# Optimization experiments

Measured on AMD Instinct MI355X. Metric: run time of the kernel, lower is better.

## Reference

```python
import jax, jax.numpy as jnp
import numpy as np

L, D, H, FF, V = 8, 768, 8, 2048, 32000
MAXLEN, TMAX = 512, 4
S = MAXLEN * TMAX  # 2048 context length
HD = D // H
EPS = 1e-4  # layer_norm_eps from module defaults


def setup_inputs() -> dict:
    key = jax.random.key(0)
    ks = jax.random.split(key, 16)
    s = 0.02
    B = 1
    rn = lambda k, shape: jax.random.normal(k, shape, jnp.float32) * s
    # sinusoidal positional encoding over MAXLEN real-token positions
    pos = np.arange(MAXLEN)[:, None]
    div = np.exp(np.arange(0, D, 2) * (-np.log(10000.0) / D))
    pe = np.zeros((MAXLEN, D), np.float32)
    pe[:, 0::2] = np.sin(pos * div)
    pe[:, 1::2] = np.cos(pos * div)
    return {
        "state_embeddings": jax.random.normal(ks[0], (B, S, D), jnp.float32),
        "padding_mask": jnp.zeros((B, S), bool),
        "pe": jnp.asarray(pe),
        "thought_emb": rn(ks[1], (TMAX, D)),
        "w_qkv": rn(ks[2], (L, 3 * D, D)),
        "b_qkv": jnp.zeros((L, 3 * D), jnp.float32),
        "w_out": rn(ks[3], (L, D, D)),
        "b_out": jnp.zeros((L, D), jnp.float32),
        "ln1_g": jnp.ones((L, D), jnp.float32),
        "ln1_b": jnp.zeros((L, D), jnp.float32),
        "ln2_g": jnp.ones((L, D), jnp.float32),
        "ln2_b": jnp.zeros((L, D), jnp.float32),
        "w_ff1": rn(ks[4], (L, FF, D)),
        "b_ff1": jnp.zeros((L, FF), jnp.float32),
        "w_ff2": rn(ks[5], (L, D, FF)),
        "b_ff2": jnp.zeros((L, D), jnp.float32),
        "fn_g": jnp.ones((D,), jnp.float32),
        "fn_b": jnp.zeros((D,), jnp.float32),
        "w_policy": rn(ks[6], (V, D)),
        "w_v1": rn(ks[7], (FF, D)),
        "b_v1": jnp.zeros((FF,), jnp.float32),
        "w_v2": rn(ks[8], (1, FF)),
        "b_v2": jnp.zeros((1,), jnp.float32),
        "n_thoughts_taken": 3,
    }


def _layer_norm(x, g, b):
    m = x.mean(-1, keepdims=True)
    v = ((x - m) ** 2).mean(-1, keepdims=True)
    return (x - m) / jnp.sqrt(v + EPS) * g + b


def reference(state_embeddings, padding_mask, pe, thought_emb, w_qkv, b_qkv, w_out, b_out, ln1_g, ln1_b, ln2_g, ln2_b, w_ff1, b_ff1, w_ff2, b_ff2, fn_g, fn_b, w_policy, w_v1, b_v1, w_v2, b_v2, n_thoughts_taken):
    tt = int(n_thoughts_taken)
    T = tt + 1  # block size (token + thoughts taken)
    B = state_embeddings.shape[0]
    R = MAXLEN  # real_token_count: all token slots real (no padding)
    # --- DualPositionalEncoding ---
    x = state_embeddings[:, :MAXLEN * T].reshape(B, MAXLEN, T, D)
    x = x + pe[None, :, None, :] + thought_emb[None, None, :T, :]
    x = x.reshape(B, MAXLEN * T, D)
    x = jnp.pad(x, ((0, 0), (0, S - MAXLEN * T), (0, 0)))
    # --- ThoughtsFormer block-causal mask (keep=True means attend) ---
    i = jnp.arange(S)
    tok, off = i // T, i % T
    same_block = (tok[:, None] == tok[None, :]) & (off[:, None] >= off[None, :]) & (tok[:, None] < R)
    global_cols = (off[None, :] == 0) & (tok[None, :] < R) & (i[:, None] > i[None, :]) & (i[:, None] < R * T)
    keep = (same_block | global_cols)[None, None] & (~padding_mask)[:, None, None, :]
    scale = 1.0 / np.sqrt(HD)

    def layer(h, p):
        wq, bq, wo, bo, g1, b1, g2, b2, wf1, bf1, wf2, bf2 = p
        # pre-norm self-attention
        y = _layer_norm(h, g1, b1)
        q, k, v = jnp.split(y @ wq.T + bq, 3, axis=-1)
        q = q.reshape(B, S, H, HD)
        k = k.reshape(B, S, H, HD)
        v = v.reshape(B, S, H, HD)
        scores = jnp.einsum('bihd,bjhd->bhij', q, k) * scale
        attn = jax.nn.softmax(jnp.where(keep, scores, -jnp.inf), axis=-1)
        o = jnp.einsum('bhij,bjhd->bihd', attn, v).reshape(B, S, D)
        h = h + o @ wo.T + bo
        # pre-norm FFN with exact (erf) GELU
        y = _layer_norm(h, g2, b2)
        h = h + jax.nn.gelu(y @ wf1.T + bf1, approximate=False) @ wf2.T + bf2
        h = jnp.where(jnp.isnan(h), 0.0, h)
        return h, None

    x, _ = jax.lax.scan(layer, x, (w_qkv, b_qkv, w_out, b_out, ln1_g, ln1_b, ln2_g, ln2_b, w_ff1, b_ff1, w_ff2, b_ff2))
    x = _layer_norm(x, fn_g, fn_b)  # TransformerEncoder final norm
    logits = x @ w_policy.T  # policy head (no bias)
    values = jax.nn.gelu(x @ w_v1.T + b_v1, approximate=False) @ w_v2.T + b_v2
    return logits, values
```

## Files before the change

### kernel.cpp

```cpp
#include <hip/hip_runtime.h>
#include <math.h>

#define S_TOT 2048
#define DMODEL 768
#define QKVD 2304
#define NHEAD 8
#define HDIM 96
#define FFDIM 2048
#define VOCAB 32000
#define MAXLEN_C 512
#define POL_CHUNK 3200
#define VLT_LD 2080
#define NEG_BIG (-3.0e38f)
#define M_INIT (-1.0e30f)
#define QK_SCALE 0.10206207261596575f

typedef __bf16 bf16x8 __attribute__((ext_vector_type(8)));
typedef float f32x4 __attribute__((ext_vector_type(4)));
typedef unsigned short u16x8 __attribute__((ext_vector_type(8)));
typedef unsigned short u16x4 __attribute__((ext_vector_type(4)));

__device__ __forceinline__ float gelu_exact(float x) {
  return 0.5f * x * (1.0f + erff(x * 0.70710678118654752f));
}

__device__ __forceinline__ float bf2f(unsigned short u) {
  union { unsigned int i; float f; } v;
  v.i = ((unsigned int)u) << 16;
  return v.f;
}

__device__ __forceinline__ unsigned short f2bf(float f) {
  union { float f; unsigned int i; } v;
  v.f = f;
  unsigned int x = v.i;
  return (unsigned short)((x + 0x7fffu + ((x >> 16) & 1u)) >> 16);
}

__device__ __forceinline__ unsigned int pack2bf(float a, float b) {
  return (unsigned int)f2bf(a) | ((unsigned int)f2bf(b) << 16);
}

__device__ __forceinline__ void gload_lds16(const unsigned short* g, unsigned short* l) {
  __builtin_amdgcn_global_load_lds(
      (const __attribute__((address_space(1))) unsigned int*)g,
      (__attribute__((address_space(3))) unsigned int*)l, 16, 0, 0);
}

__global__ __launch_bounds__(256) void embed_kernel(
    const float* __restrict__ se, const float* __restrict__ pe,
    const float* __restrict__ th, const int* __restrict__ ntt,
    float* __restrict__ X) {
  int idx = blockIdx.x * 256 + threadIdx.x;
  if (idx >= S_TOT * DMODEL) return;
  int p = idx / DMODEL;
  int d = idx - p * DMODEL;
  int T = ntt[0] + 1;
  float v = 0.0f;
  if (p < MAXLEN_C * T) {
    v = se[idx] + pe[(p / T) * DMODEL + d] + th[(p % T) * DMODEL + d];
  }
  X[idx] = v;
}

__global__ __launch_bounds__(256) void ln_bf_kernel(
    const float* __restrict__ X, const float* __restrict__ g,
    const float* __restrict__ b, unsigned short* __restrict__ Y) {
  __shared__ float red[4];
  const int row = blockIdx.x;
  const int tid = threadIdx.x;
  const float* x = X + (size_t)row * DMODEL;
  float v0 = x[tid], v1 = x[tid + 256], v2 = x[tid + 512];
  float s = v0 + v1 + v2;
  for (int o = 32; o; o >>= 1) s += __shfl_xor(s, o);
  if ((tid & 63) == 0) red[tid >> 6] = s;
  __syncthreads();
  float mean = (red[0] + red[1] + red[2] + red[3]) * (1.0f / DMODEL);
  float d0 = v0 - mean, d1 = v1 - mean, d2 = v2 - mean;
  float s2 = d0 * d0 + d1 * d1 + d2 * d2;
  for (int o = 32; o; o >>= 1) s2 += __shfl_xor(s2, o);
  __syncthreads();
  if ((tid & 63) == 0) red[tid >> 6] = s2;
  __syncthreads();
  float var = (red[0] + red[1] + red[2] + red[3]) * (1.0f / DMODEL);
  float rstd = rsqrtf(var + 1e-4f);
  unsigned short* y = Y + (size_t)row * DMODEL;
  y[tid]       = f2bf(d0 * rstd * g[tid]       + b[tid]);
  y[tid + 256] = f2bf(d1 * rstd * g[tid + 256] + b[tid + 256]);
  y[tid + 512] = f2bf(d2 * rstd * g[tid + 512] + b[tid + 512]);
}

__global__ __launch_bounds__(256) void cvt_kernel(
    const float* __restrict__ s, unsigned short* __restrict__ d, int n) {
  int i = (blockIdx.x * 256 + threadIdx.x) * 4;
  if (i >= n) return;
  float4 v = *(const float4*)(s + i);
  u16x4 o;
  o[0] = f2bf(v.x); o[1] = f2bf(v.y); o[2] = f2bf(v.z); o[3] = f2bf(v.w);
  *(u16x4*)(d + i) = o;
}

__global__ __launch_bounds__(256) void cvt4_kernel(
    const float* __restrict__ s0, const float* __restrict__ s1,
    const float* __restrict__ s2, const float* __restrict__ s3,
    unsigned short* __restrict__ d0, unsigned short* __restrict__ d1,
    unsigned short* __restrict__ d2, unsigned short* __restrict__ d3,
    int n0, int n1, int n2, int n3) {
  int i = (blockIdx.x * 256 + threadIdx.x) * 4;
  const float* s;
  unsigned short* d;
  if (i < n0) { s = s0; d = d0; }
  else if (i < n0 + n1) { i -= n0; s = s1; d = d1; }
  else if (i < n0 + n1 + n2) { i -= n0 + n1; s = s2; d = d2; }
  else if (i < n0 + n1 + n2 + n3) { i -= n0 + n1 + n2; s = s3; d = d3; }
  else return;
  float4 v = *(const float4*)(s + i);
  u16x4 o;
  o[0] = f2bf(v.x); o[1] = f2bf(v.y); o[2] = f2bf(v.z); o[3] = f2bf(v.w);
  *(u16x4*)(d + i) = o;
}

__global__ __launch_bounds__(256) void cvt6_kernel(
    const float* __restrict__ s0, const float* __restrict__ s1,
    const float* __restrict__ s2, const float* __restrict__ s3,
    const float* __restrict__ s4, const float* __restrict__ s5,
    unsigned short* __restrict__ d0, unsigned short* __restrict__ d1,
    unsigned short* __restrict__ d2, unsigned short* __restrict__ d3,
    unsigned short* __restrict__ d4, unsigned short* __restrict__ d5,
    int n0, int n1, int n2, int n3, int n4, int n5) {
  int i = (blockIdx.x * 256 + threadIdx.x) * 4;
  const float* s;
  unsigned short* d;
  if (i < n0) { s = s0; d = d0; }
  else if (i < n0 + n1) { i -= n0; s = s1; d = d1; }
  else if (i < n0 + n1 + n2) { i -= n0 + n1; s = s2; d = d2; }
  else if (i < n0 + n1 + n2 + n3) { i -= n0 + n1 + n2; s = s3; d = d3; }
  else if (i < n0 + n1 + n2 + n3 + n4) { i -= n0 + n1 + n2 + n3; s = s4; d = d4; }
  else if (i < n0 + n1 + n2 + n3 + n4 + n5) { i -= n0 + n1 + n2 + n3 + n4; s = s5; d = d5; }
  else return;
  float4 v = *(const float4*)(s + i);
  u16x4 o;
  o[0] = f2bf(v.x); o[1] = f2bf(v.y); o[2] = f2bf(v.z); o[3] = f2bf(v.w);
  *(u16x4*)(d + i) = o;
}

__global__ __launch_bounds__(256) void gemm_bf16_kernel(
    const unsigned short* __restrict__ A, const unsigned short* __restrict__ B,
    const float* __restrict__ bias, const float* __restrict__ res,
    void* __restrict__ Cout, int M, int N, int K, int ldc, int act, int outbf,
    int swiz) {
  __shared__ __align__(16) unsigned short As[2 * 4096];
  __shared__ __align__(16) unsigned short Bs[2 * 4096];
  const int t = threadIdx.x;
  const int w = t >> 6, l = t & 63;
  int n_blk, m_blk;
  if (swiz) {
    const int g = blockIdx.x;
    const int chunk = gridDim.x >> 3;
    const int logical = (g & 7) * chunk + (g >> 3);
    m_blk = logical & 15;
    n_blk = logical >> 4;
  } else {
    n_blk = blockIdx.x; m_blk = blockIdx.y;
  }
  const int n0 = n_blk * 128, i0 = m_blk * 128;
  const int wr = w >> 1, wc = w & 1;
  const int lr = l & 15;
  const int koff = (l >> 4) * 8;

  f32x4 acc[4][4] = {};

  const int srow = t >> 2;
  const int scol = (t & 3) * 8;
  const unsigned short* Ag = A + (size_t)(i0 + srow) * K + scol;
  const unsigned short* Bg = B + (size_t)(n0 + srow) * K + scol;
  const int lo0 = (w << 9);
  const int lo1 = 2048 + (w << 9);

#define STAGE128(buf, k0)                                        \
  do {                                                           \
    gload_lds16(Ag + (k0), &As[(buf) * 4096 + lo0]);             \
    gload_lds16(Ag + (size_t)64 * K + (k0), &As[(buf) * 4096 + lo1]); \
    gload_lds16(Bg + (k0), &Bs[(buf) * 4096 + lo0]);             \
    gload_lds16(Bg + (size_t)64 * K + (k0), &Bs[(buf) * 4096 + lo1]); \
  } while (0)

#define COMPUTE128(buf)                                                   \
  do {                                                                    \
    const unsigned short* Ab = &As[(buf) * 4096];                         \
    const unsigned short* Bb = &Bs[(buf) * 4096];                         \
    bf16x8 af[4], bfr[4];                                                 \
    _Pragma("unroll") for (int fi = 0; fi < 4; ++fi)                      \
        af[fi] = *(const bf16x8*)&Ab[(wr * 64 + fi * 16 + lr) * 32 + koff]; \
    _Pragma("unroll") for (int fj = 0; fj < 4; ++fj)                      \
        bfr[fj] = *(const bf16x8*)&Bb[(wc * 64 + fj * 16 + lr) * 32 + koff]; \
    _Pragma("unroll") for (int fi = 0; fi < 4; ++fi)                      \
      _Pragma("unroll") for (int fj = 0; fj < 4; ++fj)                    \
          acc[fi][fj] = __builtin_amdgcn_mfma_f32_16x16x32_bf16(          \
              bfr[fj], af[fi], acc[fi][fj], 0, 0, 0);                     \
  } while (0)

  const int nt = K >> 5;
  STAGE128(0, 0);
  int cur = 0;
  for (int tt = 0; tt < nt - 1; ++tt) {
    STAGE128(cur ^ 1, (tt + 1) << 5);
    asm volatile("s_waitcnt vmcnt(4)" ::: "memory");
    __builtin_amdgcn_s_barrier();
    __builtin_amdgcn_sched_barrier(0);
    COMPUTE128(cur);
    __builtin_amdgcn_sched_barrier(0);
    __builtin_amdgcn_s_barrier();
    cur ^= 1;
  }
  asm volatile("s_waitcnt vmcnt(0)" ::: "memory");
  __builtin_amdgcn_s_barrier();
  __builtin_amdgcn_sched_barrier(0);
  COMPUTE128(cur);

  const int mloc = l & 15, ng = (l >> 4) * 4;
#pragma unroll
  for (int fi = 0; fi < 4; ++fi) {
    const int i = i0 + wr * 64 + fi * 16 + mloc;
    const size_t rowbase = (size_t)i * ldc;
#pragma unroll
    for (int fj = 0; fj < 4; ++fj) {
      const int nb = n0 + wc * 64 + fj * 16 + ng;
      float z0 = acc[fi][fj][0], z1 = acc[fi][fj][1];
      float z2 = acc[fi][fj][2], z3 = acc[fi][fj][3];
      if (bias) {
        float4 bv = *(const float4*)(bias + nb);
        z0 += bv.x; z1 += bv.y; z2 += bv.z; z3 += bv.w;
      }
      if (act) {
        z0 = gelu_exact(z0); z1 = gelu_exact(z1);
        z2 = gelu_exact(z2); z3 = gelu_exact(z3);
      }
      if (res) {
        float4 rv = *(const float4*)(res + rowbase + nb);
        z0 += rv.x; z1 += rv.y; z2 += rv.z; z3 += rv.w;
      }
      if (outbf) {
        u16x4 o;
        o[0] = f2bf(z0); o[1] = f2bf(z1); o[2] = f2bf(z2); o[3] = f2bf(z3);
        *(u16x4*)((unsigned short*)Cout + rowbase + nb) = o;
      } else {
        *(float4*)((float*)Cout + rowbase + nb) = make_float4(z0, z1, z2, z3);
      }
    }
  }
#undef STAGE128
#undef COMPUTE128
}

__global__ __launch_bounds__(256) void gemm64_bf16_kernel(
    const unsigned short* __restrict__ A, const unsigned short* __restrict__ B,
    const float* __restrict__ bias, const float* __restrict__ res,
    void* __restrict__ Cout, int M, int N, int K, int ldc, int act, int outbf) {
  __shared__ __align__(16) unsigned short As[2 * 4096];
  __shared__ __align__(16) unsigned short Bs[2 * 4096];
  const int t = threadIdx.x;
  const int w = t >> 6, l = t & 63;
  const int n0 = blockIdx.x * 64, i0 = blockIdx.y * 64;
  const int wr = w >> 1, wc = w & 1;
  const int lr = l & 15;
  const int koff = (l >> 4) * 8;

  f32x4 acc[2][2] = {};

  const int srow = t >> 2;
  const int scol = (t & 3) * 8;
  const unsigned short* Ag = A + (size_t)(i0 + srow) * K + scol;
  const unsigned short* Bg = B + (size_t)(n0 + srow) * K + scol;
  const int lo0 = (w << 9);
  const int lo1 = 2048 + (w << 9);

#define STAGE64(buf, k0)                                      \
  do {                                                        \
    gload_lds16(Ag + (k0), &As[(buf) * 4096 + lo0]);          \
    gload_lds16(Ag + (k0) + 32, &As[(buf) * 4096 + lo1]);     \
    gload_lds16(Bg + (k0), &Bs[(buf) * 4096 + lo0]);          \
    gload_lds16(Bg + (k0) + 32, &Bs[(buf) * 4096 + lo1]);     \
  } while (0)

#define COMPUTE64(buf)                                                        \
  do {                                                                        \
    const unsigned short* Ab = &As[(buf) * 4096];                             \
    const unsigned short* Bb = &Bs[(buf) * 4096];                             \
    bf16x8 af[2][2], bfr[2][2];                                               \
    _Pragma("unroll") for (int fi = 0; fi < 2; ++fi)                          \
      _Pragma("unroll") for (int kk = 0; kk < 2; ++kk)                        \
          af[fi][kk] = *(const bf16x8*)&Ab[kk * 2048 + (wr * 32 + fi * 16 + lr) * 32 + koff]; \
    _Pragma("unroll") for (int fj = 0; fj < 2; ++fj)                          \
      _Pragma("unroll") for (int kk = 0; kk < 2; ++kk)                        \
          bfr[fj][kk] = *(const bf16x8*)&Bb[kk * 2048 + (wc * 32 + fj * 16 + lr) * 32 + koff]; \
    _Pragma("unroll") for (int fi = 0; fi < 2; ++fi)                          \
      _Pragma("unroll") for (int fj = 0; fj < 2; ++fj)                        \
        _Pragma("unroll") for (int kk = 0; kk < 2; ++kk)                      \
            acc[fi][fj] = __builtin_amdgcn_mfma_f32_16x16x32_bf16(            \
                bfr[fj][kk], af[fi][kk], acc[fi][fj], 0, 0, 0);               \
  } while (0)

  const int nt = K >> 6;
  STAGE64(0, 0);
  int cur = 0;
  for (int tt = 0; tt < nt - 1; ++tt) {
    STAGE64(cur ^ 1, (tt + 1) << 6);
    asm volatile("s_waitcnt vmcnt(4)" ::: "memory");
    __builtin_amdgcn_s_barrier();
    __builtin_amdgcn_sched_barrier(0);
    COMPUTE64(cur);
    __builtin_amdgcn_sched_barrier(0);
    __builtin_amdgcn_s_barrier();
    cur ^= 1;
  }
  asm volatile("s_waitcnt vmcnt(0)" ::: "memory");
  __builtin_amdgcn_s_barrier();
  __builtin_amdgcn_sched_barrier(0);
  COMPUTE64(cur);

  const int mloc = l & 15, ng = (l >> 4) * 4;
#pragma unroll
  for (int fi = 0; fi < 2; ++fi) {
    const int i = i0 + wr * 32 + fi * 16 + mloc;
    const size_t rowbase = (size_t)i * ldc;
#pragma unroll
    for (int fj = 0; fj < 2; ++fj) {
      const int nb = n0 + wc * 32 + fj * 16 + ng;
      float z0 = acc[fi][fj][0], z1 = acc[fi][fj][1];
      float z2 = acc[fi][fj][2], z3 = acc[fi][fj][3];
      if (bias) {
        float4 bv = *(const float4*)(bias + nb);
        z0 += bv.x; z1 += bv.y; z2 += bv.z; z3 += bv.w;
      }
      if (act) {
        z0 = gelu_exact(z0); z1 = gelu_exact(z1);
        z2 = gelu_exact(z2); z3 = gelu_exact(z3);
      }
      if (res) {
        float4 rv = *(const float4*)(res + rowbase + nb);
        z0 += rv.x; z1 += rv.y; z2 += rv.z; z3 += rv.w;
      }
      if (outbf) {
        u16x4 o;
        o[0] = f2bf(z0); o[1] = f2bf(z1); o[2] = f2bf(z2); o[3] = f2bf(z3);
        *(u16x4*)((unsigned short*)Cout + rowbase + nb) = o;
      } else {
        *(float4*)((float*)Cout + rowbase + nb) = make_float4(z0, z1, z2, z3);
      }
    }
  }
#undef STAGE64
#undef COMPUTE64
}

__global__ __launch_bounds__(256) void repack_kernel(
    const unsigned short* __restrict__ qkv, const int* __restrict__ ntt,
    unsigned short* __restrict__ Kg, unsigned short* __restrict__ Vgt,
    unsigned short* __restrict__ Vlt) {
  __shared__ unsigned short vt[64][104];
  const int pb = blockIdx.x * 64, h = blockIdx.y;
  const int T = ntt[0] + 1;
  const int tid = threadIdx.x;

  for (int idx = tid; idx < 64 * 96; idx += 256) {
    int pp = idx / 96, d = idx - pp * 96;
    vt[pp][d] = qkv[(size_t)(pb + pp) * QKVD + 2 * DMODEL + h * HDIM + d];
  }
  const int firstpp = (T - pb % T) % T;
  const int ng = (64 - firstpp + T - 1) / T;
  for (int idx = tid; idx < ng * 96; idx += 256) {
    int gi = idx / 96, d = idx - gi * 96;
    int p = pb + firstpp + gi * T;
    int g = p / T;
    if (g < MAXLEN_C)
      Kg[((size_t)h * 512 + g) * 96 + d] = qkv[(size_t)p * QKVD + DMODEL + h * HDIM + d];
  }
  __syncthreads();
  for (int idx = tid; idx < 96 * 64; idx += 256) {
    int d = idx >> 6, pp = idx & 63;
    Vlt[((size_t)h * 96 + d) * VLT_LD + pb + pp] = vt[pp][d];
  }
  for (int idx = tid; idx < ng * 96; idx += 256) {
    int d = idx / ng, gi = idx - d * ng;
    int pp = firstpp + gi * T;
    int g = (pb + pp) / T;
    if (g < MAXLEN_C && d < 96)
      Vgt[((size_t)h * 96 + d) * 512 + g] = vt[pp][d];
  }
}

__global__ __launch_bounds__(256) void attn_flash_kernel(
    const unsigned short* __restrict__ qkv, const unsigned short* __restrict__ Kg,
    const unsigned short* __restrict__ Vgt, const unsigned short* __restrict__ Vlt,
    const int* __restrict__ ntt, unsigned short* __restrict__ att) {
  __shared__ float Osh[4][96][17];
  __shared__ float Msh[4][16];
  __shared__ float Lsh[4][16];
  const int s = blockIdx.x, h = blockIdx.y;
  const int T = ntt[0] + 1;
  const int tid = threadIdx.x;
  const int w = tid >> 6, l = tid & 63;
  const int q15 = l & 15, grp = l >> 4;
  const int p0 = s * 16;
  const int p = p0 + q15;
  const int myTok = p / T;

  const unsigned short* qrow = qkv + (size_t)p * QKVD + h * HDIM + grp * 8;
  bf16x8 qf0 = *(const bf16x8*)(qrow);
  bf16x8 qf1 = *(const bf16x8*)(qrow + 32);
  bf16x8 qf2 = *(const bf16x8*)(qrow + 64);

  float m_run = M_INIT, l_run = 0.0f;
  f32x4 oacc[6] = {};

  const int gmax = (p0 + 15) / T;
  const int KP = (gmax >> 5) + 1;
  const unsigned short* KgH = Kg + (size_t)h * 512 * 96;
  const unsigned short* VgH = Vgt + (size_t)h * 96 * 512;

  for (int kp = w; kp < KP; kp += 4) {
    f32x4 s0 = {}, s1 = {};
    const unsigned short* k0r = KgH + (size_t)(kp * 32 + q15) * 96 + grp * 8;
    const unsigned short* k1r = k0r + 16 * 96;
    {
      bf16x8 a0 = *(const bf16x8*)(k0r);
      bf16x8 a1 = *(const bf16x8*)(k1r);
      bf16x8 b0 = *(const bf16x8*)(k0r + 32);
      bf16x8 b1 = *(const bf16x8*)(k1r + 32);
      bf16x8 c0 = *(const bf16x8*)(k0r + 64);
      bf16x8 c1 = *(const bf16x8*)(k1r + 64);
      __builtin_amdgcn_s_setprio(1);
      s0 = __builtin_amdgcn_mfma_f32_16x16x32_bf16(a0, qf0, s0, 0, 0, 0);
      s1 = __builtin_amdgcn_mfma_f32_16x16x32_bf16(a1, qf0, s1, 0, 0, 0);
      s0 = __builtin_amdgcn_mfma_f32_16x16x32_bf16(b0, qf1, s0, 0, 0, 0);
      s1 = __builtin_amdgcn_mfma_f32_16x16x32_bf16(b1, qf1, s1, 0, 0, 0);
      s0 = __builtin_amdgcn_mfma_f32_16x16x32_bf16(c0, qf2, s0, 0, 0, 0);
      s1 = __builtin_amdgcn_mfma_f32_16x16x32_bf16(c1, qf2, s1, 0, 0, 0);
      __builtin_amdgcn_s_setprio(0);
    }
    float sc[8];
#pragma unroll
    for (int e = 0; e < 4; ++e) {
      int g = kp * 32 + grp * 4 + e;
      sc[e] = (g * T <= p) ? s0[e] * QK_SCALE : NEG_BIG;
      g += 16;
      sc[4 + e] = (g * T <= p) ? s1[e] * QK_SCALE : NEG_BIG;
    }
    float tmax = sc[0];
#pragma unroll
    for (int e = 1; e < 8; ++e) tmax = fmaxf(tmax, sc[e]);
    tmax = fmaxf(tmax, __shfl_xor(tmax, 16));
    tmax = fmaxf(tmax, __shfl_xor(tmax, 32));
    float mnew = fmaxf(m_run, tmax);
    float alpha = __expf(m_run - mnew);
    float pv[8], ps = 0.0f;
#pragma unroll
    for (int e = 0; e < 8; ++e) { pv[e] = __expf(sc[e] - mnew); ps += pv[e]; }
    ps += __shfl_xor(ps, 16);
    ps += __shfl_xor(ps, 32);
    l_run = l_run * alpha + ps;
    m_run = mnew;
#pragma unroll
    for (int dt = 0; dt < 6; ++dt) oacc[dt] *= alpha;
    unsigned int pk0[2], pk1[2];
    pk0[0] = pack2bf(pv[0], pv[1]); pk0[1] = pack2bf(pv[2], pv[3]);
    pk1[0] = pack2bf(pv[4], pv[5]); pk1[1] = pack2bf(pv[6], pv[7]);
    union { unsigned int u[4]; bf16x8 v; } pf;
#pragma unroll
    for (int w2 = 0; w2 < 4; ++w2) {
      int src = (((grp & 1) << 1) + (w2 >> 1)) * 16 + q15;
      int y0 = __shfl((int)pk0[w2 & 1], src);
      int y1 = __shfl((int)pk1[w2 & 1], src);
      pf.u[w2] = (grp >> 1) ? (unsigned int)y1 : (unsigned int)y0;
    }
    __builtin_amdgcn_s_setprio(1);
#pragma unroll
    for (int dt = 0; dt < 6; ++dt) {
      bf16x8 vf = *(const bf16x8*)(VgH + (size_t)(dt * 16 + q15) * 512 + kp * 32 + grp * 8);
      oacc[dt] = __builtin_amdgcn_mfma_f32_16x16x32_bf16(vf, pf.v, oacc[dt], 0, 0, 0);
    }
    __builtin_amdgcn_s_setprio(0);
  }

  if (w == 3) {
    f32x4 s0 = {};
    const unsigned short* kl = qkv + (size_t)(p0 + q15) * QKVD + DMODEL + h * HDIM + grp * 8;
    __builtin_amdgcn_s_setprio(1);
    s0 = __builtin_amdgcn_mfma_f32_16x16x32_bf16(*(const bf16x8*)(kl), qf0, s0, 0, 0, 0);
    s0 = __builtin_amdgcn_mfma_f32_16x16x32_bf16(*(const bf16x8*)(kl + 32), qf1, s0, 0, 0, 0);
    s0 = __builtin_amdgcn_mfma_f32_16x16x32_bf16(*(const bf16x8*)(kl + 64), qf2, s0, 0, 0, 0);
    __builtin_amdgcn_s_setprio(0);
    float sc[4];
#pragma unroll
    for (int e = 0; e < 4; ++e) {
      int pk = p0 + grp * 4 + e;
      bool ok = (pk / T == myTok) && (pk % T != 0) && (pk <= p);
      sc[e] = ok ? s0[e] * QK_SCALE : NEG_BIG;
    }
    float tmax = fmaxf(fmaxf(sc[0], sc[1]), fmaxf(sc[2], sc[3]));
    tmax = fmaxf(tmax, __shfl_xor(tmax, 16));
    tmax = fmaxf(tmax, __shfl_xor(tmax, 32));
    float mnew = fmaxf(m_run, tmax);
    float alpha = __expf(m_run - mnew);
    float pv[4], ps = 0.0f;
#pragma unroll
    for (int e = 0; e < 4; ++e) { pv[e] = __expf(sc[e] - mnew); ps += pv[e]; }
    ps += __shfl_xor(ps, 16);
    ps += __shfl_xor(ps, 32);
    l_run = l_run * alpha + ps;
    m_run = mnew;
#pragma unroll
    for (int dt = 0; dt < 6; ++dt) oacc[dt] *= alpha;
    unsigned int pk0[2];
    pk0[0] = pack2bf(pv[0], pv[1]); pk0[1] = pack2bf(pv[2], pv[3]);
    union { unsigned int u[4]; bf16x8 v; } pf;
#pragma unroll
    for (int w2 = 0; w2 < 4; ++w2) {
      int src = (((grp & 1) << 1) + (w2 >> 1)) * 16 + q15;
      int y0 = __shfl((int)pk0[w2 & 1], src);
      pf.u[w2] = (grp >> 1) ? 0u : (unsigned int)y0;
    }
    __builtin_amdgcn_s_setprio(1);
#pragma unroll
    for (int dt = 0; dt < 6; ++dt) {
      bf16x8 vf = *(const bf16x8*)(Vlt + ((size_t)h * 96 + dt * 16 + q15) * VLT_LD + p0 + grp * 8);
      oacc[dt] = __builtin_amdgcn_mfma_f32_16x16x32_bf16(vf, pf.v, oacc[dt], 0, 0, 0);
    }
    __builtin_amdgcn_s_setprio(0);
  }

  if (l < 16) { Msh[w][l] = m_run; Lsh[w][l] = l_run; }
#pragma unroll
  for (int dt = 0; dt < 6; ++dt)
#pragma unroll
    for (int e = 0; e < 4; ++e)
      Osh[w][dt * 16 + grp * 4 + e][q15] = oacc[dt][e];
  __syncthreads();

  {
    const int q = tid & 15, dg = tid >> 4;
    float m0 = Msh[0][q], m1 = Msh[1][q], m2 = Msh[2][q], m3 = Msh[3][q];
    float ms = fmaxf(fmaxf(m0, m1), fmaxf(m2, m3));
    float c0 = __expf(m0 - ms), c1 = __expf(m1 - ms);
    float c2 = __expf(m2 - ms), c3 = __expf(m3 - ms);
    float lsum = c0 * Lsh[0][q] + c1 * Lsh[1][q] + c2 * Lsh[2][q] + c3 * Lsh[3][q];
    float rinv = 1.0f / lsum;
    unsigned short* orow = att + (size_t)(p0 + q) * DMODEL + h * HDIM;
#pragma unroll
    for (int j = 0; j < 6; ++j) {
      int d = dg * 6 + j;
      float o = c0 * Osh[0][d][q] + c1 * Osh[1][d][q] +
                c2 * Osh[2][d][q] + c3 * Osh[3][d][q];
      orow[d] = f2bf(o * rinv);
    }
  }
}

__global__ __launch_bounds__(256) void v2_kernel(
    const unsigned short* __restrict__ F1, const float* __restrict__ w2,
    const float* __restrict__ b2, float* __restrict__ out) {
  __shared__ float red[4];
  const int row = blockIdx.x;
  const int tid = threadIdx.x;
  float s = 0.0f;
  const unsigned short* xr = F1 + (size_t)row * FFDIM;
  for (int f = tid; f < FFDIM; f += 256) s += bf2f(xr[f]) * w2[f];
  for (int o = 32; o; o >>= 1) s += __shfl_xor(s, o);
  if ((tid & 63) == 0) red[tid >> 6] = s;
  __syncthreads();
  if (tid == 0) out[row] = red[0] + red[1] + red[2] + red[3] + b2[0];
}

extern "C" void kernel_launch(void* const* d_in, const int* in_sizes, int n_in,
                              void* d_out, int out_size, void* d_ws, size_t ws_size,
                              hipStream_t stream) {
  const float* se      = (const float*)d_in[0];
  const float* pe      = (const float*)d_in[2];
  const float* th      = (const float*)d_in[3];
  const float* w_qkv   = (const float*)d_in[4];
  const float* b_qkv   = (const float*)d_in[5];
  const float* w_out   = (const float*)d_in[6];
  const float* b_out   = (const float*)d_in[7];
  const float* ln1_g   = (const float*)d_in[8];
  const float* ln1_b   = (const float*)d_in[9];
  const float* ln2_g   = (const float*)d_in[10];
  const float* ln2_b   = (const float*)d_in[11];
  const float* w_ff1   = (const float*)d_in[12];
  const float* b_ff1   = (const float*)d_in[13];
  const float* w_ff2   = (const float*)d_in[14];
  const float* b_ff2   = (const float*)d_in[15];
  const float* fn_g    = (const float*)d_in[16];
  const float* fn_b    = (const float*)d_in[17];
  const float* w_pol   = (const float*)d_in[18];
  const float* w_v1    = (const float*)d_in[19];
  const float* b_v1    = (const float*)d_in[20];
  const float* w_v2    = (const float*)d_in[21];
  const float* b_v2    = (const float*)d_in[22];
  const int*   ntt     = (const int*)d_in[23];

  float* logits = (float*)d_out;
  float* values = logits + (size_t)S_TOT * VOCAB;

  const int nq = 3 * DMODEL * DMODEL, no = DMODEL * DMODEL;
  const int nf1 = FFDIM * DMODEL, nf2 = DMODEL * FFDIM;
  const int npol = VOCAB * DMODEL;

  char* p = (char*)d_ws;
  float* X             = (float*)p;          p += (size_t)S_TOT * DMODEL * 4;
  unsigned short* Ybf  = (unsigned short*)p; p += (size_t)S_TOT * DMODEL * 2;
  unsigned short* QKVb = (unsigned short*)p; p += (size_t)S_TOT * QKVD * 2;
  unsigned short* ATTb = (unsigned short*)p; p += (size_t)S_TOT * DMODEL * 2;
  unsigned short* F1b  = (unsigned short*)p; p += (size_t)S_TOT * FFDIM * 2;
  unsigned short* Kg   = (unsigned short*)p; p += (size_t)NHEAD * 512 * 96 * 2;
  unsigned short* Vgt  = (unsigned short*)p; p += (size_t)NHEAD * 96 * 512 * 2;
  unsigned short* Vlt  = (unsigned short*)p; p += (size_t)NHEAD * 96 * VLT_LD * 2;

  const size_t wbytes = ((size_t)8 * (nq + no + nf1 + nf2) + npol + nf1) * 2;
  const size_t used   = (size_t)(p - (char*)d_ws);
  const bool bigws = ws_size >= used + wbytes + (1u << 20);

  unsigned short *WqA, *WoA, *Wf1A, *Wf2A, *WpolA, *Wv1A;
  if (bigws) {
    WqA   = (unsigned short*)p; p += (size_t)8 * nq * 2;
    WoA   = (unsigned short*)p; p += (size_t)8 * no * 2;
    Wf1A  = (unsigned short*)p; p += (size_t)8 * nf1 * 2;
    Wf2A  = (unsigned short*)p; p += (size_t)8 * nf2 * 2;
    WpolA = (unsigned short*)p; p += (size_t)npol * 2;
    Wv1A  = (unsigned short*)p;
  } else {
    WqA   = (unsigned short*)p; p += (size_t)nq * 2;
    WoA   = (unsigned short*)p; p += (size_t)no * 2;
    Wf1A  = (unsigned short*)p; p += (size_t)nf1 * 2;
    Wf2A  = (unsigned short*)p; p += (size_t)nf2 * 2;
    WpolA = (unsigned short*)p;
    Wv1A  = Wf1A;
  }

  dim3 blk(256);

  if (bigws) {
    const int t0 = 8 * nq, t1 = 8 * no, t2 = 8 * nf1, t3 = 8 * nf2;
    const long total = (long)t0 + t1 + t2 + t3 + npol + nf1;
    cvt6_kernel<<<dim3((unsigned)((total / 4 + 255) / 256)), blk, 0, stream>>>(
        w_qkv, w_out, w_ff1, w_ff2, w_pol, w_v1,
        WqA, WoA, Wf1A, Wf2A, WpolA, Wv1A,
        t0, t1, t2, t3, npol, nf1);
  }

  embed_kernel<<<dim3((S_TOT * DMODEL + 255) / 256), blk, 0, stream>>>(se, pe, th, ntt, X);

  for (int l = 0; l < 8; ++l) {
    const unsigned short* pWq  = bigws ? WqA  + (size_t)l * nq  : WqA;
    const unsigned short* pWo  = bigws ? WoA  + (size_t)l * no  : WoA;
    const unsigned short* pWf1 = bigws ? Wf1A + (size_t)l * nf1 : Wf1A;
    const unsigned short* pWf2 = bigws ? Wf2A + (size_t)l * nf2 : Wf2A;
    if (!bigws) {
      const int ncvt4 = (nq + no + nf1 + nf2) / 4;
      cvt4_kernel<<<dim3((ncvt4 + 255) / 256), blk, 0, stream>>>(
          w_qkv + (size_t)l * nq, w_out + (size_t)l * no,
          w_ff1 + (size_t)l * nf1, w_ff2 + (size_t)l * nf2,
          WqA, WoA, Wf1A, Wf2A, nq, no, nf1, nf2);
    }

    ln_bf_kernel<<<dim3(S_TOT), blk, 0, stream>>>(X, ln1_g + l * DMODEL, ln1_b + l * DMODEL, Ybf);
    gemm_bf16_kernel<<<dim3(QKVD / 128, S_TOT / 128), blk, 0, stream>>>(
        Ybf, pWq, b_qkv + (size_t)l * 3 * DMODEL, nullptr, QKVb,
        S_TOT, QKVD, DMODEL, QKVD, 0, 1, 0);
    repack_kernel<<<dim3(S_TOT / 64, NHEAD), blk, 0, stream>>>(QKVb, ntt, Kg, Vgt, Vlt);
    attn_flash_kernel<<<dim3(S_TOT / 16, NHEAD), blk, 0, stream>>>(
        QKVb, Kg, Vgt, Vlt, ntt, ATTb);
    gemm64_bf16_kernel<<<dim3(DMODEL / 64, S_TOT / 64), blk, 0, stream>>>(
        ATTb, pWo, b_out + (size_t)l * DMODEL, X, X,
        S_TOT, DMODEL, DMODEL, DMODEL, 0, 0);

    ln_bf_kernel<<<dim3(S_TOT), blk, 0, stream>>>(X, ln2_g + l * DMODEL, ln2_b + l * DMODEL, Ybf);
    gemm_bf16_kernel<<<dim3(FFDIM / 128, S_TOT / 128), blk, 0, stream>>>(
        Ybf, pWf1, b_ff1 + (size_t)l * FFDIM, nullptr, F1b,
        S_TOT, FFDIM, DMODEL, FFDIM, 1, 1, 0);
    gemm64_bf16_kernel<<<dim3(DMODEL / 64, S_TOT / 64), blk, 0, stream>>>(
        F1b, pWf2, b_ff2 + (size_t)l * DMODEL, X, X,
        S_TOT, DMODEL, FFDIM, DMODEL, 0, 0);
  }

  ln_bf_kernel<<<dim3(S_TOT), blk, 0, stream>>>(X, fn_g, fn_b, Ybf);

  if (bigws) {
    gemm_bf16_kernel<<<dim3((S_TOT / 128) * (VOCAB / 128)), blk, 0, stream>>>(
        Ybf, WpolA, nullptr, nullptr, logits, S_TOT, VOCAB, DMODEL, VOCAB, 0, 0, 1);
  } else {
    for (int c = 0; c < VOCAB / POL_CHUNK; ++c) {
      cvt_kernel<<<dim3((POL_CHUNK * DMODEL / 4 + 255) / 256), blk, 0, stream>>>(
          w_pol + (size_t)c * POL_CHUNK * DMODEL, WpolA, POL_CHUNK * DMODEL);
      gemm_bf16_kernel<<<dim3(POL_CHUNK / 128, S_TOT / 128), blk, 0, stream>>>(
          Ybf, WpolA, nullptr, nullptr, logits + (size_t)c * POL_CHUNK,
          S_TOT, POL_CHUNK, DMODEL, VOCAB, 0, 0, 0);
    }
  }

  if (!bigws)
    cvt_kernel<<<dim3((nf1 / 4 + 255) / 256), blk, 0, stream>>>(w_v1, Wv1A, nf1);
  gemm_bf16_kernel<<<dim3(FFDIM / 128, S_TOT / 128), blk, 0, stream>>>(
      Ybf, Wv1A, b_v1, nullptr, F1b, S_TOT, FFDIM, DMODEL, FFDIM, 1, 1, 0);
  v2_kernel<<<dim3(S_TOT), blk, 0, stream>>>(F1b, w_v2, b_v2, values);
}
```

Baseline: 1.439 ms.

## Triple-buffer GEMM shared-memory staging and use 64-tile GEMM for QKV/FF1/value

Both bf16 GEMM kernels move from double to triple buffering in LDS, so tiles are prefetched two K-steps ahead and the vmcnt waits are adjusted to match. The QKV, FF1 and value-head GEMMs switch from the 128x128 tile kernel to the 64x64 tile kernel, which launches more workgroups on the 256-CU-class GPU. The aim is to hide global-load latency better and raise occupancy for these mid-sized GEMMs. In exchange, LDS use per block grows to 48KB, which may limit how many blocks fit per CU, and smaller tiles reload operands more often.

```diff
diff --git a/kernel.cpp b/kernel.cpp
--- a/kernel.cpp
+++ b/kernel.cpp
@@ -149,8 +149,8 @@
     const float* __restrict__ bias, const float* __restrict__ res,
     void* __restrict__ Cout, int M, int N, int K, int ldc, int act, int outbf,
     int swiz) {
-  __shared__ __align__(16) unsigned short As[2 * 4096];
-  __shared__ __align__(16) unsigned short Bs[2 * 4096];
+  __shared__ __align__(16) unsigned short As[3 * 4096];
+  __shared__ __align__(16) unsigned short Bs[3 * 4096];
   const int t = threadIdx.x;
   const int w = t >> 6, l = t & 63;
   int n_blk, m_blk;
@@ -202,21 +202,23 @@
 
   const int nt = K >> 5;
   STAGE128(0, 0);
-  int cur = 0;
-  for (int tt = 0; tt < nt - 1; ++tt) {
-    STAGE128(cur ^ 1, (tt + 1) << 5);
-    asm volatile("s_waitcnt vmcnt(4)" ::: "memory");
+  if (nt > 1) STAGE128(1, 32);
+  for (int tt = 0; tt < nt; ++tt) {
+    const int cb = tt % 3;
+    if (tt + 2 < nt) {
+      STAGE128((tt + 2) % 3, (tt + 2) << 5);
+      asm volatile("s_waitcnt vmcnt(8)" ::: "memory");
+    } else if (tt + 1 < nt) {
+      asm volatile("s_waitcnt vmcnt(4)" ::: "memory");
+    } else {
+      asm volatile("s_waitcnt vmcnt(0)" ::: "memory");
+    }
     __builtin_amdgcn_s_barrier();
     __builtin_amdgcn_sched_barrier(0);
-    COMPUTE128(cur);
+    COMPUTE128(cb);
     __builtin_amdgcn_sched_barrier(0);
     __builtin_amdgcn_s_barrier();
-    cur ^= 1;
-  }
-  asm volatile("s_waitcnt vmcnt(0)" ::: "memory");
-  __builtin_amdgcn_s_barrier();
-  __builtin_amdgcn_sched_barrier(0);
-  COMPUTE128(cur);
+  }
 
   const int mloc = l & 15, ng = (l >> 4) * 4;
 #pragma unroll
@@ -257,8 +259,8 @@
     const unsigned short* __restrict__ A, const unsigned short* __restrict__ B,
     const float* __restrict__ bias, const float* __restrict__ res,
     void* __restrict__ Cout, int M, int N, int K, int ldc, int act, int outbf) {
-  __shared__ __align__(16) unsigned short As[2 * 4096];
-  __shared__ __align__(16) unsigned short Bs[2 * 4096];
+  __shared__ __align__(16) unsigned short As[3 * 4096];
+  __shared__ __align__(16) unsigned short Bs[3 * 4096];
   const int t = threadIdx.x;
   const int w = t >> 6, l = t & 63;
   const int n0 = blockIdx.x * 64, i0 = blockIdx.y * 64;
@@ -303,21 +305,23 @@
 
   const int nt = K >> 6;
   STAGE64(0, 0);
-  int cur = 0;
-  for (int tt = 0; tt < nt - 1; ++tt) {
-    STAGE64(cur ^ 1, (tt + 1) << 6);
-    asm volatile("s_waitcnt vmcnt(4)" ::: "memory");
+  if (nt > 1) STAGE64(1, 64);
+  for (int tt = 0; tt < nt; ++tt) {
+    const int cb = tt % 3;
+    if (tt + 2 < nt) {
+      STAGE64((tt + 2) % 3, (tt + 2) << 6);
+      asm volatile("s_waitcnt vmcnt(8)" ::: "memory");
+    } else if (tt + 1 < nt) {
+      asm volatile("s_waitcnt vmcnt(4)" ::: "memory");
+    } else {
+      asm volatile("s_waitcnt vmcnt(0)" ::: "memory");
+    }
     __builtin_amdgcn_s_barrier();
     __builtin_amdgcn_sched_barrier(0);
-    COMPUTE64(cur);
+    COMPUTE64(cb);
     __builtin_amdgcn_sched_barrier(0);
     __builtin_amdgcn_s_barrier();
-    cur ^= 1;
-  }
-  asm volatile("s_waitcnt vmcnt(0)" ::: "memory");
-  __builtin_amdgcn_s_barrier();
-  __builtin_amdgcn_sched_barrier(0);
-  COMPUTE64(cur);
+  }
 
   const int mloc = l & 15, ng = (l >> 4) * 4;
 #pragma unroll
@@ -664,9 +668,9 @@
     }
 
     ln_bf_kernel<<<dim3(S_TOT), blk, 0, stream>>>(X, ln1_g + l * DMODEL, ln1_b + l * DMODEL, Ybf);
-    gemm_bf16_kernel<<<dim3(QKVD / 128, S_TOT / 128), blk, 0, stream>>>(
+    gemm64_bf16_kernel<<<dim3(QKVD / 64, S_TOT / 64), blk, 0, stream>>>(
         Ybf, pWq, b_qkv + (size_t)l * 3 * DMODEL, nullptr, QKVb,
-        S_TOT, QKVD, DMODEL, QKVD, 0, 1, 0);
+        S_TOT, QKVD, DMODEL, QKVD, 0, 1);
     repack_kernel<<<dim3(S_TOT / 64, NHEAD), blk, 0, stream>>>(QKVb, ntt, Kg, Vgt, Vlt);
     attn_flash_kernel<<<dim3(S_TOT / 16, NHEAD), blk, 0, stream>>>(
         QKVb, Kg, Vgt, Vlt, ntt, ATTb);
@@ -675,9 +679,9 @@
         S_TOT, DMODEL, DMODEL, DMODEL, 0, 0);
 
     ln_bf_kernel<<<dim3(S_TOT), blk, 0, stream>>>(X, ln2_g + l * DMODEL, ln2_b + l * DMODEL, Ybf);
-    gemm_bf16_kernel<<<dim3(FFDIM / 128, S_TOT / 128), blk, 0, stream>>>(
+    gemm64_bf16_kernel<<<dim3(FFDIM / 64, S_TOT / 64), blk, 0, stream>>>(
         Ybf, pWf1, b_ff1 + (size_t)l * FFDIM, nullptr, F1b,
-        S_TOT, FFDIM, DMODEL, FFDIM, 1, 1, 0);
+        S_TOT, FFDIM, DMODEL, FFDIM, 1, 1);
     gemm64_bf16_kernel<<<dim3(DMODEL / 64, S_TOT / 64), blk, 0, stream>>>(
         F1b, pWf2, b_ff2 + (size_t)l * DMODEL, X, X,
         S_TOT, DMODEL, FFDIM, DMODEL, 0, 0);
@@ -700,7 +704,7 @@
 
   if (!bigws)
     cvt_kernel<<<dim3((nf1 / 4 + 255) / 256), blk, 0, stream>>>(w_v1, Wv1A, nf1);
-  gemm_bf16_kernel<<<dim3(FFDIM / 128, S_TOT / 128), blk, 0, stream>>>(
-      Ybf, Wv1A, b_v1, nullptr, F1b, S_TOT, FFDIM, DMODEL, FFDIM, 1, 1, 0);
+  gemm64_bf16_kernel<<<dim3(FFDIM / 64, S_TOT / 64), blk, 0, stream>>>(
+      Ybf, Wv1A, b_v1, nullptr, F1b, S_TOT, FFDIM, DMODEL, FFDIM, 1, 1);
   v2_kernel<<<dim3(S_TOT), blk, 0, stream>>>(F1b, w_v2, b_v2, values);
 }
```

Measured after the change: 1.358 ms. 5.7% less time.
